# Performance work log

Hardware: AMD Instinct MI355X
Metric: run time of the kernel (lower is better)

The kernel has to match this reference:

```python
import jax, jax.numpy as jnp
import numpy as np

N = 8192        # number of cells/nodes
D_IN = 30       # input feature dim
P_DIM = 3       # position dim
HID = 32        # attention hidden dim
D_OUT = 30      # backbone output dim
FF = 128        # MLP hidden width
SIGMA = 0.3     # spatial decay sigma


def setup_inputs() -> dict:
    key = jax.random.key(0)
    ks = jax.random.split(key, 12)
    w = lambda k, shape: (jax.random.normal(k, shape, jnp.float32) * 0.1)
    return {
        "t": jax.random.uniform(ks[0], (1,), jnp.float32),
        "Z": jax.random.normal(ks[1], (N, D_IN + P_DIM + 1), jnp.float32),
        # SpatialAttentionLayer params (Q/K/V projections + output proj)
        "Wq": w(ks[2], (D_IN, HID)), "bq": jnp.zeros((HID,), jnp.float32),
        "Wk": w(ks[3], (D_IN, HID)), "bk": jnp.zeros((HID,), jnp.float32),
        "Wv": w(ks[4], (D_IN, HID)), "bv": jnp.zeros((HID,), jnp.float32),
        "Wo": w(ks[5], (HID, D_OUT)), "bo": jnp.zeros((D_OUT,), jnp.float32),
        # LayerNorm
        "ln_g": jnp.ones((D_OUT,), jnp.float32), "ln_b": jnp.zeros((D_OUT,), jnp.float32),
        # backbone MLP: Linear(30,128) -> SiLU -> Linear(128,30)
        "W1": w(ks[6], (D_OUT, FF)), "b1": jnp.zeros((FF,), jnp.float32),
        "W2": w(ks[7], (FF, D_OUT)), "b2": jnp.zeros((D_OUT,), jnp.float32),
        # expr_head: Linear(30,30)
        "We": w(ks[8], (D_OUT, D_OUT)), "be": jnp.zeros((D_OUT,), jnp.float32),
    }


def reference(t, Z, Wq, bq, Wk, bk, Wv, bv, Wo, bo, ln_g, ln_b, W1, b1, W2, b2, We, be):
    # Z: (N, D_IN + P_DIM + 1); last column is kinetic energy (unused in fwd)
    X = Z[:, :-1]                       # (N, 33)
    P = X[:, -P_DIM:]                   # (N, 3) positions
    F = X[:, :D_IN]                     # (N, 30) features

    # --- SpatialAttentionLayer: sigma distance-decay attention, no softmax ---
    Q = F @ Wq + bq
    K = F @ Wk + bk
    V = F @ Wv + bv
    scores = (Q @ K.T) / jnp.sqrt(jnp.float32(HID))          # (N, N)
    pn = jnp.sum(P * P, axis=1)
    d2 = jnp.maximum(pn[:, None] + pn[None, :] - 2.0 * (P @ P.T), 0.0)
    decay = jnp.exp(-d2 / (2.0 * SIGMA * SIGMA))              # spatial decay kernel
    A = jax.nn.sigmoid(scores) * decay                        # no-softmax attention
    A = A / (jnp.sum(A, axis=1, keepdims=True) + 1e-8)        # row-normalized message passing
    H = (A @ V) @ Wo + bo                                     # (N, D_OUT)

    # --- LayerNorm(output_dim) ---
    mu = jnp.mean(H, axis=-1, keepdims=True)
    var = jnp.mean((H - mu) ** 2, axis=-1, keepdims=True)
    Hn = (H - mu) * jax.lax.rsqrt(var + 1e-5) * ln_g + ln_b

    # --- Linear(30,128) -> SiLU -> Linear(128,30) ---
    H2 = jax.nn.silu(Hn @ W1 + b1) @ W2 + b2

    # --- expr_head ---
    feature_velo = H2 @ We + be                               # (N, 30)

    # static_pos=True -> zero position velocities (velocity_head bypassed)
    pos_velo = jnp.zeros_like(P)                              # (N, 3)

    # kinetic energy term
    ke = 0.5 * jnp.mean(feature_velo ** 2, axis=1) + 0.5 * jnp.mean(pos_velo ** 2, axis=1)
    return jnp.concatenate([feature_velo, pos_velo, ke[:, None]], axis=1)  # (N, 34)
```

## Files before the change

### kernel.cpp

```cpp
#include <hip/hip_runtime.h>
#include <hip/hip_bf16.h>

#define N      8192
#define D_IN   30
#define HID    32
#define D_OUT  30
#define FFD    128
#define ZC     34
#define JGC    16
#define NCH    4

typedef __attribute__((ext_vector_type(8))) short short8;
typedef __attribute__((ext_vector_type(16))) float f32x16;

static __device__ __forceinline__ ushort f2bf(float x) {
    uint32_t u = __float_as_uint(x);
    uint32_t r = (u + 0x7fffu + ((u >> 16) & 1u)) >> 16;
    return (ushort)r;
}
static __device__ __forceinline__ float bf2f(ushort u) {
    return __uint_as_float(((uint32_t)u) << 16);
}
static __device__ __forceinline__ float rdlane(float v, int l) {
    return __uint_as_float(__builtin_amdgcn_readlane(__float_as_uint(v), l));
}

__global__ __launch_bounds__(256) void dv_qkv_kernel(
    const float* __restrict__ Z,
    const float* __restrict__ Wq, const float* __restrict__ bq,
    const float* __restrict__ Wk, const float* __restrict__ bk,
    const float* __restrict__ Wv, const float* __restrict__ bv,
    const float* __restrict__ Wo,
    const float* __restrict__ W2, const float* __restrict__ We,
    const float* __restrict__ b2, const float* __restrict__ be,
    ushort* __restrict__ Qb, ushort* __restrict__ Kb,
    ushort* __restrict__ VWot, ushort* __restrict__ KA,
    ushort* __restrict__ QB, float* __restrict__ W2e, float* __restrict__ b2e)
{
    __shared__ ushort sv[8][33];
    const int t = blockIdx.x * 256 + threadIdx.x;
    const int i = t >> 5;
    const int h = t & 31;
    const float* z = Z + (size_t)i * ZC;

    float q = bq[h], k = bk[h], v = bv[h];
#pragma unroll
    for (int d = 0; d < D_IN; ++d) {
        float zf = z[d];
        q = fmaf(zf, Wq[d * HID + h], q);
        k = fmaf(zf, Wk[d * HID + h], k);
        v = fmaf(zf, Wv[d * HID + h], v);
    }
    const float QS = 0.17677669529663687f * 1.4426950408889634f;
    Qb[(size_t)i * HID + h] = f2bf(q * QS);
    Kb[(size_t)i * HID + h] = f2bf(k);
    sv[threadIdx.x >> 5][h] = f2bf(v);

    if (h == 0) {
        float p0 = z[D_IN], p1 = z[D_IN + 1], p2 = z[D_IN + 2];
        const float C2 = 1.4426950408889634f / 0.18f;
        const float SC = sqrtf(2.0f * C2);
        float px = p0 * SC, py = p1 * SC, pz = p2 * SC;
        float w  = -C2 * (p0 * p0 + p1 * p1 + p2 * p2);
        ushort phx = f2bf(px), phy = f2bf(py), phz = f2bf(pz);
        ushort plx = f2bf(px - bf2f(phx));
        ushort ply = f2bf(py - bf2f(phy));
        ushort plz = f2bf(pz - bf2f(phz));
        ushort wh  = f2bf(w);
        ushort wl  = f2bf(w - bf2f(wh));
        ushort nhx = phx ^ 0x8000, nhy = phy ^ 0x8000, nhz = phz ^ 0x8000;
        ushort nlx = plx ^ 0x8000, nly = ply ^ 0x8000, nlz = plz ^ 0x8000;
        ushort nwh = wh ^ 0x8000,  nwl = wl ^ 0x8000;
        const ushort one = 0x3F80, none = 0xBF80;
        ushort ka0[8] = {nwh, nwl, none, none, nhx, nhy, nhz, nhx};
        ushort ka1[8] = {nhy, nhz, nlx, nly, nlz, nlx, nly, nlz};
        ushort qb0[8] = {one, one, wh, wl, phx, phy, phz, plx};
        ushort qb1[8] = {ply, plz, phx, phy, phz, plx, ply, plz};
        *(uint4*)&KA[(size_t)i * 8]       = *(uint4*)ka0;
        *(uint4*)&KA[((size_t)N + i) * 8] = *(uint4*)ka1;
        *(uint4*)&QB[(size_t)i * 8]       = *(uint4*)qb0;
        *(uint4*)&QB[((size_t)N + i) * 8] = *(uint4*)qb1;
    }

    if (blockIdx.x < 15) {
        int idx = blockIdx.x * 256 + threadIdx.x;
        int f = idx / 30, o = idx - f * 30;
        float acc = 0.f;
#pragma unroll
        for (int d = 0; d < D_OUT; ++d)
            acc = fmaf(W2[f * D_OUT + d], We[d * D_OUT + o], acc);
        W2e[idx] = acc;
        if (idx < D_OUT) {
            float a2 = be[idx];
#pragma unroll
            for (int d = 0; d < D_OUT; ++d)
                a2 = fmaf(b2[d], We[d * D_OUT + idx], a2);
            b2e[idx] = a2;
        }
    }

    __syncthreads();
    const int io = threadIdx.x >> 5, c = threadIdx.x & 31;
    const int ii = blockIdx.x * 8 + io;
    float val;
    if (c < 30) {
        float acc = 0.f;
#pragma unroll
        for (int hh = 0; hh < HID; ++hh)
            acc = fmaf(bf2f(sv[io][hh]), Wo[hh * D_OUT + c], acc);
        val = acc;
    } else {
        val = (c == 31) ? 1.0f : 0.f;
    }
    VWot[(size_t)c * N + ii] = f2bf(val);
}

__global__ __launch_bounds__(256, 2) void dv_attn_kernel(
    const ushort* __restrict__ Qb, const ushort* __restrict__ Kb,
    const ushort* __restrict__ VWot, const ushort* __restrict__ KA,
    const ushort* __restrict__ QB, ushort* __restrict__ partial)
{
    __shared__ ushort lK[2][128 * 32];
    __shared__ ushort lV[2][32 * 128];
    __shared__ ushort lKA[2][2][128 * 8];

    const int tid  = threadIdx.x;
    const int lane = tid & 63;
    const int wv   = tid >> 6;
    const int h2   = lane >> 5;
    const int l31  = lane & 31;
    const int rb   = blockIdx.x & 63;
    const int jg   = blockIdx.x >> 6;
    const int i0w  = rb * 128 + wv * 32;

    const ushort* qp = Qb + (size_t)(i0w + l31) * HID + h2 * 8;
    const short8 qf0 = *(const short8*)qp;
    const short8 qf1 = *(const short8*)(qp + 16);
    const short8 qaug = *(const short8*)&QB[((size_t)h2 * N + i0w + l31) * 8];

    f32x16 zacc, oacc;
#pragma unroll
    for (int r = 0; r < 16; ++r) { zacc[r] = 0.f; oacc[r] = 0.f; }

    const int cA0 = (h2 + (l31 >> 1)) & 3;
    const int cA1 = (cA0 + 2) & 3;

    const int kjr0 = tid >> 2,          kcc0 = tid & 3;
    const int kjr1 = (tid + 256) >> 2,  kcc1 = (tid + 256) & 3;
    const int kc20 = (kcc0 + (kjr0 >> 1)) & 3;
    const int kc21 = (kcc1 + (kjr1 >> 1)) & 3;
    const int vhh[4] = { tid >> 5, (tid + 256) >> 5, (tid + 512) >> 5, (tid + 768) >> 5 };
    const int vcx = tid & 31;
    const int ahalf = tid >> 7, ajj = tid & 127;

    uint4 kreg[2];
    uint2 vreg[4];
    uint4 kareg;

    auto LOADC = [&](int c) {
        const int j0 = (jg * NCH + c) << 7;
        kreg[0] = *(const uint4*)&Kb[(size_t)(j0 + kjr0) * HID + kcc0 * 8];
        kreg[1] = *(const uint4*)&Kb[(size_t)(j0 + kjr1) * HID + kcc1 * 8];
#pragma unroll
        for (int r2 = 0; r2 < 4; ++r2)
            vreg[r2] = *(const uint2*)&VWot[(size_t)vhh[r2] * N + j0 + vcx * 4];
        kareg = *(const uint4*)&KA[((size_t)ahalf * N + j0 + ajj) * 8];
    };
    auto WRITEC = [&](int b) {
        *(uint4*)&lK[b][kjr0 * 32 + kc20 * 8] = kreg[0];
        *(uint4*)&lK[b][kjr1 * 32 + kc21 * 8] = kreg[1];
#pragma unroll
        for (int r2 = 0; r2 < 4; ++r2)
            *(uint2*)&lV[b][vhh[r2] * 128 + (vcx ^ vhh[r2]) * 4] = vreg[r2];
        *(uint4*)&lKA[b][ahalf][ajj * 8] = kareg;
    };

    LOADC(0);
    WRITEC(0);

#pragma unroll
    for (int ch = 0; ch < NCH; ++ch) {
        const int cur = ch & 1;
        if (ch + 1 < NCH) LOADC(ch + 1);
        __syncthreads();

        __builtin_amdgcn_s_setprio(1);
#pragma unroll
        for (int t32 = 0; t32 < 4; ++t32) {
            const ushort* krow = &lK[cur][(t32 * 32 + l31) * 32];
            short8 kf0 = *(const short8*)&krow[cA0 * 8];
            short8 kf1 = *(const short8*)&krow[cA1 * 8];
            f32x16 s = __builtin_amdgcn_mfma_f32_32x32x16_bf16(kf0, qf0, zacc, 0, 0, 0);
            s = __builtin_amdgcn_mfma_f32_32x32x16_bf16(kf1, qf1, s, 0, 0, 0);

            short8 kaug = *(const short8*)&lKA[cur][h2][(t32 * 32 + l31) * 8];
            f32x16 gA = __builtin_amdgcn_mfma_f32_32x32x16_bf16(kaug, qaug, zacc, 0, 0, 0);

            uint32_t pk[8];
#pragma unroll
            for (int p = 0; p < 8; ++p) {
                float eg0 = __builtin_amdgcn_exp2f(-gA[2 * p]);
                float es0 = __builtin_amdgcn_exp2f(-s[2 * p]);
                float a0  = eg0 * __builtin_amdgcn_rcpf(1.0f + es0);
                float eg1 = __builtin_amdgcn_exp2f(-gA[2 * p + 1]);
                float es1 = __builtin_amdgcn_exp2f(-s[2 * p + 1]);
                float a1  = eg1 * __builtin_amdgcn_rcpf(1.0f + es1);
                asm("v_cvt_pk_bf16_f32 %0, %1, %2" : "=v"(pk[p]) : "v"(a0), "v"(a1));
            }
            union BV { uint32_t u[4]; short8 v; };
            BV fa, fb;
            fa.u[0] = pk[0]; fa.u[1] = pk[1]; fa.u[2] = pk[2]; fa.u[3] = pk[3];
            fb.u[0] = pk[4]; fb.u[1] = pk[5]; fb.u[2] = pk[6]; fb.u[3] = pk[7];

            const ushort* vrow = &lV[cur][l31 * 128];
            const int cb = t32 * 8 + h2;
            BV b0, b1;
            *(uint2*)&b0.u[0] = *(const uint2*)&vrow[((cb    ) ^ l31) * 4];
            *(uint2*)&b0.u[2] = *(const uint2*)&vrow[((cb + 2) ^ l31) * 4];
            *(uint2*)&b1.u[0] = *(const uint2*)&vrow[((cb + 4) ^ l31) * 4];
            *(uint2*)&b1.u[2] = *(const uint2*)&vrow[((cb + 6) ^ l31) * 4];

            oacc = __builtin_amdgcn_mfma_f32_32x32x16_bf16(fa.v, b0.v, oacc, 0, 0, 0);
            oacc = __builtin_amdgcn_mfma_f32_32x32x16_bf16(fb.v, b1.v, oacc, 0, 0, 0);
        }
        __builtin_amdgcn_s_setprio(0);

        if (ch + 1 < NCH) WRITEC(cur ^ 1);
    }

#pragma unroll
    for (int r = 0; r < 16; ++r) {
        int ir = (r & 3) + 8 * (r >> 2) + 4 * h2 + i0w;
        partial[(size_t)ir * (JGC * 32) + jg * 32 + l31] = f2bf(oacc[r]);
    }
}

__global__ __launch_bounds__(256) void dv_epilogue_kernel(
    const ushort* __restrict__ partial,
    const float* __restrict__ bo,
    const float* __restrict__ ln_g, const float* __restrict__ ln_b,
    const float* __restrict__ W1, const float* __restrict__ b1,
    const float* __restrict__ W2e, const float* __restrict__ b2e,
    float* __restrict__ out)
{
    __shared__ float shf[4][FFD];

    const int tid  = threadIdx.x;
    const int wv   = tid >> 6;
    const int lane = tid & 63;
    const int row  = blockIdx.x * 4 + wv;
    const int c    = lane & 31;
    const int half = lane >> 5;
    const bool a30 = c < 30;
    const int  c30 = a30 ? c : 0;

    float s8 = 0.f;
    {
        const ushort* pp = partial + (size_t)row * (JGC * 32) + lane;
#pragma unroll
        for (int q = 0; q < 8; ++q) s8 += bf2f(pp[q * 64]);
    }
    float sv = s8 + __shfl_xor(s8, 32, 64);

    float rsum = __shfl(sv, 31, 32);
    float inv  = __builtin_amdgcn_rcpf(rsum + 1e-8f);
    float Hl   = a30 ? fmaf(sv, inv, bo[c30]) : 0.f;

    float x = Hl;
#pragma unroll
    for (int m = 1; m < 32; m <<= 1) x += __shfl_xor(x, m, 32);
    float mu = x * (1.0f / D_OUT);
    float d  = a30 ? (Hl - mu) : 0.f;
    float v2 = d * d;
#pragma unroll
    for (int m = 1; m < 32; m <<= 1) v2 += __shfl_xor(v2, m, 32);
    float rs = rsqrtf(v2 * (1.0f / D_OUT) + 1e-5f);
    float Hn = fmaf(d * rs, ln_g[c30], ln_b[c30]);

    float acc0 = b1[lane], acc1 = b1[lane + 64];
#pragma unroll
    for (int o = 0; o < D_OUT; ++o) {
        float ho = rdlane(Hn, o);
        acc0 = fmaf(ho, W1[o * FFD + lane], acc0);
        acc1 = fmaf(ho, W1[o * FFD + lane + 64], acc1);
    }
    const float L2E = 1.4426950408889634f;
    shf[wv][lane] =
        acc0 * __builtin_amdgcn_rcpf(1.0f + __builtin_amdgcn_exp2f(-acc0 * L2E));
    shf[wv][lane + 64] =
        acc1 * __builtin_amdgcn_rcpf(1.0f + __builtin_amdgcn_exp2f(-acc1 * L2E));

    float acc = 0.f;
    {
        const float* hbase = &shf[wv][half * 64];
#pragma unroll
        for (int k = 0; k < 16; ++k) {
            float4 hv = *(const float4*)&hbase[k * 4];
            const int f0 = half * 64 + k * 4;
            acc = fmaf(hv.x, W2e[(f0    ) * D_OUT + c30], acc);
            acc = fmaf(hv.y, W2e[(f0 + 1) * D_OUT + c30], acc);
            acc = fmaf(hv.z, W2e[(f0 + 2) * D_OUT + c30], acc);
            acc = fmaf(hv.w, W2e[(f0 + 3) * D_OUT + c30], acc);
        }
    }
    float val = acc + __shfl_xor(acc, 32, 64) + b2e[c30];

    if (lane < 32 && a30)
        out[(size_t)row * ZC + c] = val;

    float kep = (a30 && half == 0) ? val * val : 0.f;
#pragma unroll
    for (int m = 1; m < 32; m <<= 1) kep += __shfl_xor(kep, m, 32);
    if (lane == 0) {
        float* op = out + (size_t)row * ZC;
        op[30] = 0.f; op[31] = 0.f; op[32] = 0.f;
        op[33] = kep * (0.5f / D_OUT);
    }
}

extern "C" void kernel_launch(void* const* d_in, const int* in_sizes, int n_in,
                              void* d_out, int out_size, void* d_ws, size_t ws_size,
                              hipStream_t stream)
{
    const float* Z  = (const float*)d_in[1];
    const float* Wq = (const float*)d_in[2];
    const float* bq = (const float*)d_in[3];
    const float* Wk = (const float*)d_in[4];
    const float* bk = (const float*)d_in[5];
    const float* Wv = (const float*)d_in[6];
    const float* bv = (const float*)d_in[7];
    const float* Wo = (const float*)d_in[8];
    const float* bo = (const float*)d_in[9];
    const float* lg = (const float*)d_in[10];
    const float* lb = (const float*)d_in[11];
    const float* W1 = (const float*)d_in[12];
    const float* b1 = (const float*)d_in[13];
    const float* W2 = (const float*)d_in[14];
    const float* b2 = (const float*)d_in[15];
    const float* We = (const float*)d_in[16];
    const float* be = (const float*)d_in[17];
    float* out = (float*)d_out;

    ushort* Qb   = (ushort*)d_ws;
    ushort* Kb   = Qb + (size_t)N * HID;
    ushort* VWot = Kb + (size_t)N * HID;
    ushort* KA   = VWot + (size_t)N * HID;
    ushort* QB   = KA + (size_t)N * 16;
    float*  W2e  = (float*)(QB + (size_t)N * 16);
    float*  b2e  = W2e + FFD * D_OUT;
    ushort* partial = (ushort*)(b2e + 32);

    hipLaunchKernelGGL(dv_qkv_kernel, dim3((N * HID) / 256), dim3(256), 0, stream,
                       Z, Wq, bq, Wk, bk, Wv, bv, Wo, W2, We, b2, be,
                       Qb, Kb, VWot, KA, QB, W2e, b2e);
    hipLaunchKernelGGL(dv_attn_kernel, dim3(64 * JGC), dim3(256), 0, stream,
                       Qb, Kb, VWot, KA, QB, partial);
    hipLaunchKernelGGL(dv_epilogue_kernel, dim3(N / 4), dim3(256), 0, stream,
                       partial, bo, lg, lb, W1, b1, W2e, b2e, out);
}
```

Before: 55.40 us.

## Process two query row tiles per wave to reuse K/V LDS loads

```diff
diff --git a/kernel.cpp b/kernel.cpp
--- a/kernel.cpp
+++ b/kernel.cpp
@@ -129,18 +129,23 @@
     const int wv   = tid >> 6;
     const int h2   = lane >> 5;
     const int l31  = lane & 31;
-    const int rb   = blockIdx.x & 63;
-    const int jg   = blockIdx.x >> 6;
-    const int i0w  = rb * 128 + wv * 32;
-
-    const ushort* qp = Qb + (size_t)(i0w + l31) * HID + h2 * 8;
-    const short8 qf0 = *(const short8*)qp;
-    const short8 qf1 = *(const short8*)(qp + 16);
-    const short8 qaug = *(const short8*)&QB[((size_t)h2 * N + i0w + l31) * 8];
-
-    f32x16 zacc, oacc;
-#pragma unroll
-    for (int r = 0; r < 16; ++r) { zacc[r] = 0.f; oacc[r] = 0.f; }
+    const int rb   = blockIdx.x & 31;
+    const int jg   = blockIdx.x >> 5;
+    const int i0A  = rb * 256 + wv * 32;
+    const int i0B  = i0A + 128;
+
+    const ushort* qpA = Qb + (size_t)(i0A + l31) * HID + h2 * 8;
+    const short8 qf0A = *(const short8*)qpA;
+    const short8 qf1A = *(const short8*)(qpA + 16);
+    const short8 qaugA = *(const short8*)&QB[((size_t)h2 * N + i0A + l31) * 8];
+    const ushort* qpB = Qb + (size_t)(i0B + l31) * HID + h2 * 8;
+    const short8 qf0B = *(const short8*)qpB;
+    const short8 qf1B = *(const short8*)(qpB + 16);
+    const short8 qaugB = *(const short8*)&QB[((size_t)h2 * N + i0B + l31) * 8];
+
+    f32x16 zacc, oaccA, oaccB;
+#pragma unroll
+    for (int r = 0; r < 16; ++r) { zacc[r] = 0.f; oaccA[r] = 0.f; oaccB[r] = 0.f; }
 
     const int cA0 = (h2 + (l31 >> 1)) & 3;
     const int cA1 = (cA0 + 2) & 3;
@@ -190,27 +195,39 @@
             const ushort* krow = &lK[cur][(t32 * 32 + l31) * 32];
             short8 kf0 = *(const short8*)&krow[cA0 * 8];
             short8 kf1 = *(const short8*)&krow[cA1 * 8];
-            f32x16 s = __builtin_amdgcn_mfma_f32_32x32x16_bf16(kf0, qf0, zacc, 0, 0, 0);
-            s = __builtin_amdgcn_mfma_f32_32x32x16_bf16(kf1, qf1, s, 0, 0, 0);
-
             short8 kaug = *(const short8*)&lKA[cur][h2][(t32 * 32 + l31) * 8];
-            f32x16 gA = __builtin_amdgcn_mfma_f32_32x32x16_bf16(kaug, qaug, zacc, 0, 0, 0);
-
-            uint32_t pk[8];
+
+            f32x16 sA = __builtin_amdgcn_mfma_f32_32x32x16_bf16(kf0, qf0A, zacc, 0, 0, 0);
+            f32x16 sB = __builtin_amdgcn_mfma_f32_32x32x16_bf16(kf0, qf0B, zacc, 0, 0, 0);
+            sA = __builtin_amdgcn_mfma_f32_32x32x16_bf16(kf1, qf1A, sA, 0, 0, 0);
+            sB = __builtin_amdgcn_mfma_f32_32x32x16_bf16(kf1, qf1B, sB, 0, 0, 0);
+            f32x16 gAA = __builtin_amdgcn_mfma_f32_32x32x16_bf16(kaug, qaugA, zacc, 0, 0, 0);
+            f32x16 gAB = __builtin_amdgcn_mfma_f32_32x32x16_bf16(kaug, qaugB, zacc, 0, 0, 0);
+
+            uint32_t pkA[8], pkB[8];
 #pragma unroll
             for (int p = 0; p < 8; ++p) {
-                float eg0 = __builtin_amdgcn_exp2f(-gA[2 * p]);
-                float es0 = __builtin_amdgcn_exp2f(-s[2 * p]);
-                float a0  = eg0 * __builtin_amdgcn_rcpf(1.0f + es0);
-                float eg1 = __builtin_amdgcn_exp2f(-gA[2 * p + 1]);
-                float es1 = __builtin_amdgcn_exp2f(-s[2 * p + 1]);
-                float a1  = eg1 * __builtin_amdgcn_rcpf(1.0f + es1);
-                asm("v_cvt_pk_bf16_f32 %0, %1, %2" : "=v"(pk[p]) : "v"(a0), "v"(a1));
+                float egA0 = __builtin_amdgcn_exp2f(-gAA[2 * p]);
+                float esA0 = __builtin_amdgcn_exp2f(-sA[2 * p]);
+                float aA0  = egA0 * __builtin_amdgcn_rcpf(1.0f + esA0);
+                float egA1 = __builtin_amdgcn_exp2f(-gAA[2 * p + 1]);
+                float esA1 = __builtin_amdgcn_exp2f(-sA[2 * p + 1]);
+                float aA1  = egA1 * __builtin_amdgcn_rcpf(1.0f + esA1);
+                asm("v_cvt_pk_bf16_f32 %0, %1, %2" : "=v"(pkA[p]) : "v"(aA0), "v"(aA1));
+                float egB0 = __builtin_amdgcn_exp2f(-gAB[2 * p]);
+                float esB0 = __builtin_amdgcn_exp2f(-sB[2 * p]);
+                float aB0  = egB0 * __builtin_amdgcn_rcpf(1.0f + esB0);
+                float egB1 = __builtin_amdgcn_exp2f(-gAB[2 * p + 1]);
+                float esB1 = __builtin_amdgcn_exp2f(-sB[2 * p + 1]);
+                float aB1  = egB1 * __builtin_amdgcn_rcpf(1.0f + esB1);
+                asm("v_cvt_pk_bf16_f32 %0, %1, %2" : "=v"(pkB[p]) : "v"(aB0), "v"(aB1));
             }
             union BV { uint32_t u[4]; short8 v; };
-            BV fa, fb;
-            fa.u[0] = pk[0]; fa.u[1] = pk[1]; fa.u[2] = pk[2]; fa.u[3] = pk[3];
-            fb.u[0] = pk[4]; fb.u[1] = pk[5]; fb.u[2] = pk[6]; fb.u[3] = pk[7];
+            BV faA, fbA, faB, fbB;
+            faA.u[0] = pkA[0]; faA.u[1] = pkA[1]; faA.u[2] = pkA[2]; faA.u[3] = pkA[3];
+            fbA.u[0] = pkA[4]; fbA.u[1] = pkA[5]; fbA.u[2] = pkA[6]; fbA.u[3] = pkA[7];
+            faB.u[0] = pkB[0]; faB.u[1] = pkB[1]; faB.u[2] = pkB[2]; faB.u[3] = pkB[3];
+            fbB.u[0] = pkB[4]; fbB.u[1] = pkB[5]; fbB.u[2] = pkB[6]; fbB.u[3] = pkB[7];
 
             const ushort* vrow = &lV[cur][l31 * 128];
             const int cb = t32 * 8 + h2;
@@ -220,8 +237,10 @@
             *(uint2*)&b1.u[0] = *(const uint2*)&vrow[((cb + 4) ^ l31) * 4];
             *(uint2*)&b1.u[2] = *(const uint2*)&vrow[((cb + 6) ^ l31) * 4];
 
-            oacc = __builtin_amdgcn_mfma_f32_32x32x16_bf16(fa.v, b0.v, oacc, 0, 0, 0);
-            oacc = __builtin_amdgcn_mfma_f32_32x32x16_bf16(fb.v, b1.v, oacc, 0, 0, 0);
+            oaccA = __builtin_amdgcn_mfma_f32_32x32x16_bf16(faA.v, b0.v, oaccA, 0, 0, 0);
+            oaccB = __builtin_amdgcn_mfma_f32_32x32x16_bf16(faB.v, b0.v, oaccB, 0, 0, 0);
+            oaccA = __builtin_amdgcn_mfma_f32_32x32x16_bf16(fbA.v, b1.v, oaccA, 0, 0, 0);
+            oaccB = __builtin_amdgcn_mfma_f32_32x32x16_bf16(fbB.v, b1.v, oaccB, 0, 0, 0);
         }
         __builtin_amdgcn_s_setprio(0);
 
@@ -230,8 +249,9 @@
 
 #pragma unroll
     for (int r = 0; r < 16; ++r) {
-        int ir = (r & 3) + 8 * (r >> 2) + 4 * h2 + i0w;
-        partial[(size_t)ir * (JGC * 32) + jg * 32 + l31] = f2bf(oacc[r]);
+        int ro = (r & 3) + 8 * (r >> 2) + 4 * h2;
+        partial[(size_t)(i0A + ro) * (JGC * 32) + jg * 32 + l31] = f2bf(oaccA[r]);
+        partial[(size_t)(i0B + ro) * (JGC * 32) + jg * 32 + l31] = f2bf(oaccB[r]);
     }
 }
 
@@ -353,7 +373,7 @@
     hipLaunchKernelGGL(dv_qkv_kernel, dim3((N * HID) / 256), dim3(256), 0, stream,
                        Z, Wq, bq, Wk, bk, Wv, bv, Wo, W2, We, b2, be,
                        Qb, Kb, VWot, KA, QB, W2e, b2e);
-    hipLaunchKernelGGL(dv_attn_kernel, dim3(64 * JGC), dim3(256), 0, stream,
+    hipLaunchKernelGGL(dv_attn_kernel, dim3(32 * JGC), dim3(256), 0, stream,
                        Qb, Kb, VWot, KA, QB, partial);
     hipLaunchKernelGGL(dv_epilogue_kernel, dim3(N / 4), dim3(256), 0, stream,
                        partial, bo, lg, lb, W1, b1, W2e, b2e, out);
```

Result: no change. 55.75 us (+0.6%).
